# Kernel optimization log

Measured on AMD Instinct MI355X. Metric: run time of the kernel, lower is better.

The kernel has to match this reference:

```python
import jax, jax.numpy as jnp
import numpy as np

N_NODES = 40000
N_EDGES = 640000
D = 128
BN_EPS = 1e-5


def setup_inputs() -> dict:
    key = jax.random.key(0)
    ks = jax.random.split(key, 8)
    h = jax.random.normal(ks[0], (N_NODES, D), dtype=jnp.float32)
    snorm_n = jax.random.uniform(ks[1], (N_NODES, 1), dtype=jnp.float32)
    W_self = jax.random.normal(ks[2], (D, D), dtype=jnp.float32) * 0.05
    W_neigh = jax.random.normal(ks[3], (D, D), dtype=jnp.float32) * 0.05
    b = jax.random.normal(ks[4], (D,), dtype=jnp.float32) * 0.05
    gamma = jnp.ones((D,), dtype=jnp.float32)
    beta = jnp.zeros((D,), dtype=jnp.float32)
    src = jax.random.randint(ks[5], (N_EDGES,), 0, N_NODES, dtype=jnp.int32)
    dst = jax.random.randint(ks[6], (N_EDGES,), 0, N_NODES, dtype=jnp.int32)
    return {"h": h, "snorm_n": snorm_n, "W_self": W_self, "W_neigh": W_neigh,
            "b": b, "gamma": gamma, "beta": beta, "src": src, "dst": dst}


def reference(h, snorm_n, W_self, W_neigh, b, gamma, beta, src, dst):
    h_in = h
    # --- SAGEConv (mean aggregator): mean over in-neighbors (src -> dst) ---
    msg = h[src]                                   # [E, D] irregular gather
    agg = jax.ops.segment_sum(msg, dst, num_segments=N_NODES)  # [N, D]
    deg = jax.ops.segment_sum(jnp.ones((N_EDGES,), h.dtype), dst,
                              num_segments=N_NODES)            # [N]
    h_neigh = agg / jnp.maximum(deg, 1.0)[:, None]
    out = h @ W_self + h_neigh @ W_neigh + b       # fc_self + fc_neigh + bias
    out = jax.nn.relu(out)                         # activation
    # --- graph norm ---
    out = out * snorm_n
    # --- batch norm (training-style batch statistics over nodes) ---
    mean = jnp.mean(out, axis=0)
    var = jnp.var(out, axis=0)
    out = (out - mean) * jax.lax.rsqrt(var + BN_EPS) * gamma + beta
    # --- residual ---
    return h_in + out
```

## Files before the change

kernel.cpp:

```cpp
#include <hip/hip_runtime.h>
#include <hip/hip_bf16.h>

constexpr int N_NODES = 40000;
constexpr int N_EDGES = 640000;
constexpr int D = 128;
constexpr float BN_EPS = 1e-5f;
constexpr int CAP = 128;
constexpr int NTILES = 1250;
constexpr int NCOLOR = 8;
constexpr int NODES_PER_COLOR = N_NODES / NCOLOR;
constexpr int FILL_BLOCKS = 2560;
constexpr int COLOR_STRIDE = (FILL_BLOCKS / NCOLOR) * 256;

typedef __attribute__((ext_vector_type(8))) short short8;
typedef __attribute__((ext_vector_type(4))) float f32x4;
typedef __attribute__((ext_vector_type(2))) float f32x2;

__device__ __forceinline__ unsigned bf16_rne(float f) {
    unsigned b = __float_as_uint(f);
    return (b + 0x7FFFu + ((b >> 16) & 1u)) >> 16;
}
__device__ __forceinline__ float bflo(unsigned w) { return __uint_as_float(w << 16); }
__device__ __forceinline__ float bfhi(unsigned w) { return __uint_as_float(w & 0xFFFF0000u); }

__global__ __launch_bounds__(256) void cvt_fill_kernel(
        const int* __restrict__ dst,
        const int* __restrict__ src,
        int* __restrict__ cursor,
        int* __restrict__ esrc,
        const float4* __restrict__ h4,
        uint4* __restrict__ hb4,
        uint2* __restrict__ hb8,
        const float* __restrict__ Wself,
        const float* __restrict__ Wneigh,
        uint4* __restrict__ wfrag) {
    int gid = blockIdx.x * blockDim.x + threadIdx.x;

    if (gid < N_EDGES) {
        float4 a = h4[2 * gid];
        float4 b = h4[2 * gid + 1];
        uint4 o;
        o.x = bf16_rne(a.x) | (bf16_rne(a.y) << 16);
        o.y = bf16_rne(a.z) | (bf16_rne(a.w) << 16);
        o.z = bf16_rne(b.x) | (bf16_rne(b.y) << 16);
        o.w = bf16_rne(b.z) | (bf16_rne(b.w) << 16);
        hb4[gid] = o;
        unsigned w0 = __builtin_amdgcn_cvt_pk_fp8_f32(a.x, a.y, 0, false);
        w0 = __builtin_amdgcn_cvt_pk_fp8_f32(a.z, a.w, w0, true);
        unsigned w1 = __builtin_amdgcn_cvt_pk_fp8_f32(b.x, b.y, 0, false);
        w1 = __builtin_amdgcn_cvt_pk_fp8_f32(b.z, b.w, w1, true);
        uint2 o8; o8.x = w0; o8.y = w1;
        hb8[gid] = o8;
    }
    if (gid < 4096) {
        int G = gid;
        int l = G & 63;
        int tile = G >> 6;
        int kg = l >> 4, n = l & 15;
        int ct = tile >> 3, kt = tile & 7;
        int k0 = kt * 32 + kg * 8;
        int col = ct * 16 + n;
        unsigned w[8];
        #pragma unroll
        for (int j = 0; j < 8; j++) {
            int k = k0 + j;
            float v = (k < D) ? Wself[(size_t)k * D + col]
                              : Wneigh[(size_t)(k - D) * D + col];
            w[j] = bf16_rne(v);
        }
        uint4 ow;
        ow.x = w[0] | (w[1] << 16);
        ow.y = w[2] | (w[3] << 16);
        ow.z = w[4] | (w[5] << 16);
        ow.w = w[6] | (w[7] << 16);
        wfrag[G] = ow;
    }

    int c = blockIdx.x & (NCOLOR - 1);
    int lo = c * NODES_PER_COLOR;
    int hi = lo + NODES_PER_COLOR;
    int base = (blockIdx.x >> 3) * 256 + threadIdx.x;
    for (int e = base; e < N_EDGES; e += COLOR_STRIDE) {
        int t = dst[e];
        if (t >= lo && t < hi) {
            int s = src[e];
            int p = atomicAdd(&cursor[t], 1);
            if (p < CAP) esrc[t * CAP + p] = s;
        }
    }
}

__global__ __launch_bounds__(256) void gather_kernel(
        const uint4* __restrict__ hb8q,
        const int* __restrict__ cursor,
        const int* __restrict__ esrc,
        uint4* __restrict__ hnb4) {
    int c = blockIdx.x & (NCOLOR - 1);
    int rank = blockIdx.x >> 3;
    int wid = threadIdx.x >> 6;
    int node = c * NODES_PER_COLOR + rank * 4 + wid;
    int lane = threadIdx.x & 63;
    int g  = lane & 7;
    int es = lane >> 3;
    int deg = cursor[node];
    int cnt = deg < CAP ? deg : CAP;
    const int* bucket = esrc + node * CAP;
    float acc[16];
    #pragma unroll
    for (int i = 0; i < 16; i++) acc[i] = 0.f;
    for (int j = es; j < cnt; j += 8) {
        int a = bucket[j];
        uint4 v = hb8q[(size_t)a * 8 + g];
        f32x2 f;
        f = __builtin_amdgcn_cvt_pk_f32_fp8(v.x, false); acc[0]  += f.x; acc[1]  += f.y;
        f = __builtin_amdgcn_cvt_pk_f32_fp8(v.x, true);  acc[2]  += f.x; acc[3]  += f.y;
        f = __builtin_amdgcn_cvt_pk_f32_fp8(v.y, false); acc[4]  += f.x; acc[5]  += f.y;
        f = __builtin_amdgcn_cvt_pk_f32_fp8(v.y, true);  acc[6]  += f.x; acc[7]  += f.y;
        f = __builtin_amdgcn_cvt_pk_f32_fp8(v.z, false); acc[8]  += f.x; acc[9]  += f.y;
        f = __builtin_amdgcn_cvt_pk_f32_fp8(v.z, true);  acc[10] += f.x; acc[11] += f.y;
        f = __builtin_amdgcn_cvt_pk_f32_fp8(v.w, false); acc[12] += f.x; acc[13] += f.y;
        f = __builtin_amdgcn_cvt_pk_f32_fp8(v.w, true);  acc[14] += f.x; acc[15] += f.y;
    }
    #pragma unroll
    for (int i = 0; i < 16; i++) {
        acc[i] += __shfl_xor(acc[i], 8);
        acc[i] += __shfl_xor(acc[i], 16);
        acc[i] += __shfl_xor(acc[i], 32);
    }
    if (es == 0) {
        float rd = 1.0f / (float)(deg > 1 ? deg : 1);
        uint4 o0, o1;
        o0.x = bf16_rne(acc[0] * rd)  | (bf16_rne(acc[1] * rd)  << 16);
        o0.y = bf16_rne(acc[2] * rd)  | (bf16_rne(acc[3] * rd)  << 16);
        o0.z = bf16_rne(acc[4] * rd)  | (bf16_rne(acc[5] * rd)  << 16);
        o0.w = bf16_rne(acc[6] * rd)  | (bf16_rne(acc[7] * rd)  << 16);
        o1.x = bf16_rne(acc[8] * rd)  | (bf16_rne(acc[9] * rd)  << 16);
        o1.y = bf16_rne(acc[10] * rd) | (bf16_rne(acc[11] * rd) << 16);
        o1.z = bf16_rne(acc[12] * rd) | (bf16_rne(acc[13] * rd) << 16);
        o1.w = bf16_rne(acc[14] * rd) | (bf16_rne(acc[15] * rd) << 16);
        hnb4[(size_t)node * 16 + g * 2]     = o0;
        hnb4[(size_t)node * 16 + g * 2 + 1] = o1;
    }
}

__global__ __launch_bounds__(256) void gemm_kernel(
        const uint4* __restrict__ hb4,
        const uint4* __restrict__ hnb4,
        const uint4* __restrict__ wfrag,
        const float* __restrict__ snorm,
        const float* __restrict__ bias,
        ushort* __restrict__ preb,
        float* __restrict__ sums,
        float* __restrict__ sumsq) {
    __shared__ uint4 ldsW[2048];
    __shared__ float sums_l[64];
    __shared__ float sumsq_l[64];

    int t = threadIdx.x;
    int lane = t & 63;
    int wid = t >> 6;
    int n = lane & 15;
    int kg = lane >> 4;
    int rowtile = blockIdx.x >> 1;
    int cbt = blockIdx.x & 1;
    int cb = cbt * 64;
    int row_base = rowtile * 64 + wid * 16;
    int row = row_base + n;

    if (t < 64) { sums_l[t] = 0.f; sumsq_l[t] = 0.f; }

    short8 a[8];
    #pragma unroll
    for (int kt = 0; kt < 4; kt++) {
        uint4 v = hb4[(size_t)row * 16 + kt * 4 + kg];
        a[kt] = __builtin_bit_cast(short8, v);
    }
    #pragma unroll
    for (int kt = 0; kt < 4; kt++) {
        uint4 v = hnb4[(size_t)row * 16 + kt * 4 + kg];
        a[4 + kt] = __builtin_bit_cast(short8, v);
    }

    #pragma unroll
    for (int i = 0; i < 8; i++) {
        int g = i * 256 + t;
        ldsW[g] = wfrag[cbt * 2048 + g];
    }
    __syncthreads();

    f32x4 acc[4];
    #pragma unroll
    for (int lt = 0; lt < 4; lt++) acc[lt] = (f32x4){0.f, 0.f, 0.f, 0.f};
    #pragma unroll
    for (int lt = 0; lt < 4; lt++) {
        #pragma unroll
        for (int kt = 0; kt < 8; kt++) {
            short8 b = __builtin_bit_cast(short8, ldsW[(lt * 8 + kt) * 64 + lane]);
            acc[lt] = __builtin_amdgcn_mfma_f32_16x16x32_bf16(a[kt], b, acc[lt], 0, 0, 0);
        }
    }

    float snv[4];
    #pragma unroll
    for (int r = 0; r < 4; r++) snv[r] = snorm[row_base + kg * 4 + r];

    #pragma unroll
    for (int lt = 0; lt < 4; lt++) {
        int col = cb + lt * 16 + n;
        float bb = bias[col];
        float csum = 0.f, csq = 0.f;
        #pragma unroll
        for (int r = 0; r < 4; r++) {
            int rr = row_base + kg * 4 + r;
            float v = acc[lt][r] + bb;
            v = fmaxf(v, 0.f);
            v *= snv[r];
            preb[(size_t)rr * D + col] = (ushort)bf16_rne(v);
            csum += v;
            csq += v * v;
        }
        csum += __shfl_xor(csum, 16); csq += __shfl_xor(csq, 16);
        csum += __shfl_xor(csum, 32); csq += __shfl_xor(csq, 32);
        if (kg == 0) {
            atomicAdd(&sums_l[lt * 16 + n], csum);
            atomicAdd(&sumsq_l[lt * 16 + n], csq);
        }
    }
    __syncthreads();
    if (t < 64) {
        atomicAdd(&sums[cb + t], sums_l[t]);
        atomicAdd(&sumsq[cb + t], sumsq_l[t]);
    }
}

__global__ __launch_bounds__(256) void final_kernel(
        const float4* __restrict__ h4,
        const float4* __restrict__ sums4,
        const float4* __restrict__ sumsq4,
        const float4* __restrict__ gamma4,
        const float4* __restrict__ beta4,
        const uint4* __restrict__ preb4,
        float4* __restrict__ out4) {
    int idx = blockIdx.x * blockDim.x + threadIdx.x;
    int total = N_NODES * D / 8;
    if (idx >= total) return;
    int g = idx & 15;
    const float invN = 1.0f / (float)N_NODES;

    float4 s0 = sums4[2 * g],  s1 = sums4[2 * g + 1];
    float4 q0 = sumsq4[2 * g], q1 = sumsq4[2 * g + 1];
    float4 g0 = gamma4[2 * g], g1 = gamma4[2 * g + 1];
    float4 b0 = beta4[2 * g],  b1 = beta4[2 * g + 1];

    uint4 p = preb4[idx];
    float4 h0 = h4[2 * idx], h1 = h4[2 * idx + 1];
    float4 o0, o1;
    float m, var, sc;

    m = s0.x * invN; var = q0.x * invN - m * m; sc = g0.x * rsqrtf(var + BN_EPS);
    o0.x = h0.x + (bflo(p.x) - m) * sc + b0.x;
    m = s0.y * invN; var = q0.y * invN - m * m; sc = g0.y * rsqrtf(var + BN_EPS);
    o0.y = h0.y + (bfhi(p.x) - m) * sc + b0.y;
    m = s0.z * invN; var = q0.z * invN - m * m; sc = g0.z * rsqrtf(var + BN_EPS);
    o0.z = h0.z + (bflo(p.y) - m) * sc + b0.z;
    m = s0.w * invN; var = q0.w * invN - m * m; sc = g0.w * rsqrtf(var + BN_EPS);
    o0.w = h0.w + (bfhi(p.y) - m) * sc + b0.w;

    m = s1.x * invN; var = q1.x * invN - m * m; sc = g1.x * rsqrtf(var + BN_EPS);
    o1.x = h1.x + (bflo(p.z) - m) * sc + b1.x;
    m = s1.y * invN; var = q1.y * invN - m * m; sc = g1.y * rsqrtf(var + BN_EPS);
    o1.y = h1.y + (bfhi(p.z) - m) * sc + b1.y;
    m = s1.z * invN; var = q1.z * invN - m * m; sc = g1.z * rsqrtf(var + BN_EPS);
    o1.z = h1.z + (bflo(p.w) - m) * sc + b1.z;
    m = s1.w * invN; var = q1.w * invN - m * m; sc = g1.w * rsqrtf(var + BN_EPS);
    o1.w = h1.w + (bfhi(p.w) - m) * sc + b1.w;

    out4[2 * idx]     = o0;
    out4[2 * idx + 1] = o1;
}

extern "C" void kernel_launch(void* const* d_in, const int* in_sizes, int n_in,
                              void* d_out, int out_size, void* d_ws, size_t ws_size,
                              hipStream_t stream) {
    const float* h      = (const float*)d_in[0];
    const float* snorm  = (const float*)d_in[1];
    const float* Wself  = (const float*)d_in[2];
    const float* Wneigh = (const float*)d_in[3];
    const float* bias   = (const float*)d_in[4];
    const float* gamma  = (const float*)d_in[5];
    const float* beta   = (const float*)d_in[6];
    const int*   src    = (const int*)d_in[7];
    const int*   dst    = (const int*)d_in[8];
    float* out = (float*)d_out;

    int*   cursor = (int*)d_ws;
    float* sums   = (float*)(cursor + N_NODES);
    float* sumsq  = sums + D;
    int*   esrc   = (int*)(sumsq + D);
    size_t off    = (size_t)((char*)(esrc + (size_t)N_NODES * CAP) - (char*)d_ws);
    off = (off + 15) & ~(size_t)15;
    uint4* wfrag = (uint4*)((char*)d_ws + off);
    uint4* hb4   = wfrag + 4096;
    uint4* hnb4  = hb4 + N_NODES * (D / 8);
    ushort* preb = (ushort*)(hnb4 + N_NODES * (D / 8));
    uint2* hb8   = (uint2*)(preb + (size_t)N_NODES * D);

    size_t zero_bytes = (size_t)(N_NODES + 2 * D) * sizeof(float);
    hipMemsetAsync(d_ws, 0, zero_bytes, stream);

    cvt_fill_kernel<<<FILL_BLOCKS, 256, 0, stream>>>(
        dst, src, cursor, esrc, (const float4*)h, hb4, hb8, Wself, Wneigh, wfrag);
    gather_kernel<<<N_NODES / 4, 256, 0, stream>>>(
        (const uint4*)hb8, cursor, esrc, hnb4);
    gemm_kernel<<<NTILES, 256, 0, stream>>>(hb4, hnb4, wfrag, snorm, bias,
                                            preb, sums, sumsq);
    final_kernel<<<(N_NODES * D / 8 + 255) / 256, 256, 0, stream>>>(
        (const float4*)h, (const float4*)sums, (const float4*)sumsq,
        (const float4*)gamma, (const float4*)beta, (const uint4*)preb,
        (float4*)out);
}
```

Measured before the change: 172.7 us.

## Fuse neighbor gather into GEMM kernel via swizzled LDS tile

Merges the mean-aggregation gather and the dual GEMM into one kernel. Each block of 64 rows first gathers its neighbor means into a swizzled LDS tile, then runs MFMA over both 64-column halves of the output, reloading W fragments between halves. This removes the global round trip of the aggregated tensor and one launch. The cost is fewer blocks (625 instead of 1250 GEMM blocks and 10000 gather blocks), so there is less parallelism to hide the irregular gather latency, and the color-based node ordering is lost.

```diff
diff --git a/kernel.cpp b/kernel.cpp
--- a/kernel.cpp
+++ b/kernel.cpp
@@ -6,11 +6,11 @@
 constexpr int D = 128;
 constexpr float BN_EPS = 1e-5f;
 constexpr int CAP = 128;
-constexpr int NTILES = 1250;
 constexpr int NCOLOR = 8;
 constexpr int NODES_PER_COLOR = N_NODES / NCOLOR;
 constexpr int FILL_BLOCKS = 2560;
 constexpr int COLOR_STRIDE = (FILL_BLOCKS / NCOLOR) * 256;
+constexpr int GG_BLOCKS = N_NODES / 64;
 
 typedef __attribute__((ext_vector_type(8))) short short8;
 typedef __attribute__((ext_vector_type(4))) float f32x4;
@@ -90,62 +90,11 @@
     }
 }
 
-__global__ __launch_bounds__(256) void gather_kernel(
+__global__ __launch_bounds__(256) void gemm_gather_kernel(
+        const uint4* __restrict__ hb4,
         const uint4* __restrict__ hb8q,
         const int* __restrict__ cursor,
         const int* __restrict__ esrc,
-        uint4* __restrict__ hnb4) {
-    int c = blockIdx.x & (NCOLOR - 1);
-    int rank = blockIdx.x >> 3;
-    int wid = threadIdx.x >> 6;
-    int node = c * NODES_PER_COLOR + rank * 4 + wid;
-    int lane = threadIdx.x & 63;
-    int g  = lane & 7;
-    int es = lane >> 3;
-    int deg = cursor[node];
-    int cnt = deg < CAP ? deg : CAP;
-    const int* bucket = esrc + node * CAP;
-    float acc[16];
-    #pragma unroll
-    for (int i = 0; i < 16; i++) acc[i] = 0.f;
-    for (int j = es; j < cnt; j += 8) {
-        int a = bucket[j];
-        uint4 v = hb8q[(size_t)a * 8 + g];
-        f32x2 f;
-        f = __builtin_amdgcn_cvt_pk_f32_fp8(v.x, false); acc[0]  += f.x; acc[1]  += f.y;
-        f = __builtin_amdgcn_cvt_pk_f32_fp8(v.x, true);  acc[2]  += f.x; acc[3]  += f.y;
-        f = __builtin_amdgcn_cvt_pk_f32_fp8(v.y, false); acc[4]  += f.x; acc[5]  += f.y;
-        f = __builtin_amdgcn_cvt_pk_f32_fp8(v.y, true);  acc[6]  += f.x; acc[7]  += f.y;
-        f = __builtin_amdgcn_cvt_pk_f32_fp8(v.z, false); acc[8]  += f.x; acc[9]  += f.y;
-        f = __builtin_amdgcn_cvt_pk_f32_fp8(v.z, true);  acc[10] += f.x; acc[11] += f.y;
-        f = __builtin_amdgcn_cvt_pk_f32_fp8(v.w, false); acc[12] += f.x; acc[13] += f.y;
-        f = __builtin_amdgcn_cvt_pk_f32_fp8(v.w, true);  acc[14] += f.x; acc[15] += f.y;
-    }
-    #pragma unroll
-    for (int i = 0; i < 16; i++) {
-        acc[i] += __shfl_xor(acc[i], 8);
-        acc[i] += __shfl_xor(acc[i], 16);
-        acc[i] += __shfl_xor(acc[i], 32);
-    }
-    if (es == 0) {
-        float rd = 1.0f / (float)(deg > 1 ? deg : 1);
-        uint4 o0, o1;
-        o0.x = bf16_rne(acc[0] * rd)  | (bf16_rne(acc[1] * rd)  << 16);
-        o0.y = bf16_rne(acc[2] * rd)  | (bf16_rne(acc[3] * rd)  << 16);
-        o0.z = bf16_rne(acc[4] * rd)  | (bf16_rne(acc[5] * rd)  << 16);
-        o0.w = bf16_rne(acc[6] * rd)  | (bf16_rne(acc[7] * rd)  << 16);
-        o1.x = bf16_rne(acc[8] * rd)  | (bf16_rne(acc[9] * rd)  << 16);
-        o1.y = bf16_rne(acc[10] * rd) | (bf16_rne(acc[11] * rd) << 16);
-        o1.z = bf16_rne(acc[12] * rd) | (bf16_rne(acc[13] * rd) << 16);
-        o1.w = bf16_rne(acc[14] * rd) | (bf16_rne(acc[15] * rd) << 16);
-        hnb4[(size_t)node * 16 + g * 2]     = o0;
-        hnb4[(size_t)node * 16 + g * 2 + 1] = o1;
-    }
-}
-
-__global__ __launch_bounds__(256) void gemm_kernel(
-        const uint4* __restrict__ hb4,
-        const uint4* __restrict__ hnb4,
         const uint4* __restrict__ wfrag,
         const float* __restrict__ snorm,
         const float* __restrict__ bias,
@@ -153,50 +102,110 @@
         float* __restrict__ sums,
         float* __restrict__ sumsq) {
     __shared__ uint4 ldsW[2048];
-    __shared__ float sums_l[64];
-    __shared__ float sumsq_l[64];
+    __shared__ uint4 ntile[1024];
+    __shared__ float sums_l[128];
+    __shared__ float sumsq_l[128];
 
     int t = threadIdx.x;
     int lane = t & 63;
     int wid = t >> 6;
-    int n = lane & 15;
+    int row_base = blockIdx.x * 64 + wid * 16;
+
+    if (t < 128) { sums_l[t] = 0.f; sumsq_l[t] = 0.f; }
+
+    #pragma unroll
+    for (int i = 0; i < 8; i++) ldsW[i * 256 + t] = wfrag[i * 256 + t];
+
+    int g  = lane & 7;
+    int es = lane >> 3;
+    for (int i = 0; i < 16; i++) {
+        int node = row_base + i;
+        int deg = cursor[node];
+        int cnt = deg < CAP ? deg : CAP;
+        const int* bucket = esrc + node * CAP;
+        float acc[16];
+        #pragma unroll
+        for (int q = 0; q < 16; q++) acc[q] = 0.f;
+        for (int j = es; j < cnt; j += 8) {
+            int a = bucket[j];
+            uint4 v = hb8q[(size_t)a * 8 + g];
+            f32x2 f;
+            f = __builtin_amdgcn_cvt_pk_f32_fp8(v.x, false); acc[0]  += f.x; acc[1]  += f.y;
+            f = __builtin_amdgcn_cvt_pk_f32_fp8(v.x, true);  acc[2]  += f.x; acc[3]  += f.y;
+            f = __builtin_amdgcn_cvt_pk_f32_fp8(v.y, false); acc[4]  += f.x; acc[5]  += f.y;
+            f = __builtin_amdgcn_cvt_pk_f32_fp8(v.y, true);  acc[6]  += f.x; acc[7]  += f.y;
+            f = __builtin_amdgcn_cvt_pk_f32_fp8(v.z, false); acc[8]  += f.x; acc[9]  += f.y;
+            f = __builtin_amdgcn_cvt_pk_f32_fp8(v.z, true);  acc[10] += f.x; acc[11] += f.y;
+            f = __builtin_amdgcn_cvt_pk_f32_fp8(v.w, false); acc[12] += f.x; acc[13] += f.y;
+            f = __builtin_amdgcn_cvt_pk_f32_fp8(v.w, true);  acc[14] += f.x; acc[15] += f.y;
+        }
+        #pragma unroll
+        for (int q = 0; q < 16; q++) {
+            acc[q] += __shfl_xor(acc[q], 8);
+            acc[q] += __shfl_xor(acc[q], 16);
+            acc[q] += __shfl_xor(acc[q], 32);
+        }
+        if (es == 0) {
+            float rd = 1.0f / (float)(deg > 1 ? deg : 1);
+            uint4 o0, o1;
+            o0.x = bf16_rne(acc[0] * rd)  | (bf16_rne(acc[1] * rd)  << 16);
+            o0.y = bf16_rne(acc[2] * rd)  | (bf16_rne(acc[3] * rd)  << 16);
+            o0.z = bf16_rne(acc[4] * rd)  | (bf16_rne(acc[5] * rd)  << 16);
+            o0.w = bf16_rne(acc[6] * rd)  | (bf16_rne(acc[7] * rd)  << 16);
+            o1.x = bf16_rne(acc[8] * rd)  | (bf16_rne(acc[9] * rd)  << 16);
+            o1.y = bf16_rne(acc[10] * rd) | (bf16_rne(acc[11] * rd) << 16);
+            o1.z = bf16_rne(acc[12] * rd) | (bf16_rne(acc[13] * rd) << 16);
+            o1.w = bf16_rne(acc[14] * rd) | (bf16_rne(acc[15] * rd) << 16);
+            int rloc = wid * 16 + i;
+            int base = rloc * 16;
+            int sw = rloc & 7;
+            ntile[base + ((g * 2)     ^ sw)] = o0;
+            ntile[base + ((g * 2 + 1) ^ sw)] = o1;
+        }
+    }
+    __syncthreads();
+
+    int n  = lane & 15;
     int kg = lane >> 4;
-    int rowtile = blockIdx.x >> 1;
-    int cbt = blockIdx.x & 1;
-    int cb = cbt * 64;
-    int row_base = rowtile * 64 + wid * 16;
     int row = row_base + n;
 
-    if (t < 64) { sums_l[t] = 0.f; sumsq_l[t] = 0.f; }
-
-    short8 a[8];
-    #pragma unroll
-    for (int kt = 0; kt < 4; kt++) {
-        uint4 v = hb4[(size_t)row * 16 + kt * 4 + kg];
-        a[kt] = __builtin_bit_cast(short8, v);
-    }
-    #pragma unroll
-    for (int kt = 0; kt < 4; kt++) {
-        uint4 v = hnb4[(size_t)row * 16 + kt * 4 + kg];
-        a[4 + kt] = __builtin_bit_cast(short8, v);
-    }
-
-    #pragma unroll
-    for (int i = 0; i < 8; i++) {
-        int g = i * 256 + t;
-        ldsW[g] = wfrag[cbt * 2048 + g];
-    }
-    __syncthreads();
-
-    f32x4 acc[4];
-    #pragma unroll
-    for (int lt = 0; lt < 4; lt++) acc[lt] = (f32x4){0.f, 0.f, 0.f, 0.f};
+    uint4 a_s[4], a_n[4];
+    #pragma unroll
+    for (int kt = 0; kt < 4; kt++)
+        a_s[kt] = hb4[(size_t)row * 16 + kt * 4 + kg];
+    {
+        int rloc = wid * 16 + n;
+        int base = rloc * 16;
+        int sw = rloc & 7;
+        #pragma unroll
+        for (int kt = 0; kt < 4; kt++)
+            a_n[kt] = ntile[base + ((kt * 4 + kg) ^ sw)];
+    }
+
+    f32x4 acc8[8];
+    #pragma unroll
+    for (int q = 0; q < 8; q++) acc8[q] = (f32x4){0.f, 0.f, 0.f, 0.f};
+
     #pragma unroll
     for (int lt = 0; lt < 4; lt++) {
         #pragma unroll
         for (int kt = 0; kt < 8; kt++) {
             short8 b = __builtin_bit_cast(short8, ldsW[(lt * 8 + kt) * 64 + lane]);
-            acc[lt] = __builtin_amdgcn_mfma_f32_16x16x32_bf16(a[kt], b, acc[lt], 0, 0, 0);
+            short8 a = __builtin_bit_cast(short8, (kt < 4) ? a_s[kt] : a_n[kt - 4]);
+            acc8[lt] = __builtin_amdgcn_mfma_f32_16x16x32_bf16(a, b, acc8[lt], 0, 0, 0);
+        }
+    }
+    __syncthreads();
+    #pragma unroll
+    for (int i = 0; i < 8; i++) ldsW[i * 256 + t] = wfrag[2048 + i * 256 + t];
+    __syncthreads();
+    #pragma unroll
+    for (int lt = 0; lt < 4; lt++) {
+        #pragma unroll
+        for (int kt = 0; kt < 8; kt++) {
+            short8 b = __builtin_bit_cast(short8, ldsW[(lt * 8 + kt) * 64 + lane]);
+            short8 a = __builtin_bit_cast(short8, (kt < 4) ? a_s[kt] : a_n[kt - 4]);
+            acc8[4 + lt] = __builtin_amdgcn_mfma_f32_16x16x32_bf16(a, b, acc8[4 + lt], 0, 0, 0);
         }
     }
 
@@ -205,31 +214,34 @@
     for (int r = 0; r < 4; r++) snv[r] = snorm[row_base + kg * 4 + r];
 
     #pragma unroll
-    for (int lt = 0; lt < 4; lt++) {
-        int col = cb + lt * 16 + n;
-        float bb = bias[col];
-        float csum = 0.f, csq = 0.f;
-        #pragma unroll
-        for (int r = 0; r < 4; r++) {
-            int rr = row_base + kg * 4 + r;
-            float v = acc[lt][r] + bb;
-            v = fmaxf(v, 0.f);
-            v *= snv[r];
-            preb[(size_t)rr * D + col] = (ushort)bf16_rne(v);
-            csum += v;
-            csq += v * v;
-        }
-        csum += __shfl_xor(csum, 16); csq += __shfl_xor(csq, 16);
-        csum += __shfl_xor(csum, 32); csq += __shfl_xor(csq, 32);
-        if (kg == 0) {
-            atomicAdd(&sums_l[lt * 16 + n], csum);
-            atomicAdd(&sumsq_l[lt * 16 + n], csq);
+    for (int hh = 0; hh < 2; hh++) {
+        #pragma unroll
+        for (int lt = 0; lt < 4; lt++) {
+            int col = hh * 64 + lt * 16 + n;
+            float bb = bias[col];
+            float csum = 0.f, csq = 0.f;
+            #pragma unroll
+            for (int r = 0; r < 4; r++) {
+                int rr = row_base + kg * 4 + r;
+                float v = acc8[hh * 4 + lt][r] + bb;
+                v = fmaxf(v, 0.f);
+                v *= snv[r];
+                preb[(size_t)rr * D + col] = (ushort)bf16_rne(v);
+                csum += v;
+                csq += v * v;
+            }
+            csum += __shfl_xor(csum, 16); csq += __shfl_xor(csq, 16);
+            csum += __shfl_xor(csum, 32); csq += __shfl_xor(csq, 32);
+            if (kg == 0) {
+                atomicAdd(&sums_l[col], csum);
+                atomicAdd(&sumsq_l[col], csq);
+            }
         }
     }
     __syncthreads();
-    if (t < 64) {
-        atomicAdd(&sums[cb + t], sums_l[t]);
-        atomicAdd(&sumsq[cb + t], sumsq_l[t]);
+    if (t < 128) {
+        atomicAdd(&sums[t], sums_l[t]);
+        atomicAdd(&sumsq[t], sumsq_l[t]);
     }
 }
 
@@ -301,8 +313,7 @@
     off = (off + 15) & ~(size_t)15;
     uint4* wfrag = (uint4*)((char*)d_ws + off);
     uint4* hb4   = wfrag + 4096;
-    uint4* hnb4  = hb4 + N_NODES * (D / 8);
-    ushort* preb = (ushort*)(hnb4 + N_NODES * (D / 8));
+    ushort* preb = (ushort*)(hb4 + N_NODES * (D / 8));
     uint2* hb8   = (uint2*)(preb + (size_t)N_NODES * D);
 
     size_t zero_bytes = (size_t)(N_NODES + 2 * D) * sizeof(float);
@@ -310,10 +321,9 @@
 
     cvt_fill_kernel<<<FILL_BLOCKS, 256, 0, stream>>>(
         dst, src, cursor, esrc, (const float4*)h, hb4, hb8, Wself, Wneigh, wfrag);
-    gather_kernel<<<N_NODES / 4, 256, 0, stream>>>(
-        (const uint4*)hb8, cursor, esrc, hnb4);
-    gemm_kernel<<<NTILES, 256, 0, stream>>>(hb4, hnb4, wfrag, snorm, bias,
-                                            preb, sums, sumsq);
+    gemm_gather_kernel<<<GG_BLOCKS, 256, 0, stream>>>(
+        hb4, (const uint4*)hb8, cursor, esrc, wfrag, snorm, bias,
+        preb, sums, sumsq);
     final_kernel<<<(N_NODES * D / 8 + 255) / 256, 256, 0, stream>>>(
         (const float4*)h, (const float4*)sums, (const float4*)sumsq,
         (const float4*)gamma, (const float4*)beta, (const uint4*)preb,
```

New measurement: 184.1 us. 6.6% more time.
